# Kernel tuning notes

Measured on AMD Instinct MI355X. Metric: run time of the kernel, lower is better.

## Reference

```python
import jax, jax.numpy as jnp
import numpy as np


def _lerp_idx(in_size, out_size):
    # align_corners=True mapping: src = dst * (in-1)/(out-1)
    pos = jnp.arange(out_size, dtype=jnp.float32) * ((in_size - 1) / (out_size - 1))
    i0 = jnp.clip(jnp.floor(pos).astype(jnp.int32), 0, in_size - 2)
    w = pos - i0.astype(jnp.float32)
    return i0, i0 + 1, w


def _upsample_bilinear_ac(x, scale):
    # x: [B,C,H,W] -> [B,C,H*scale,W*scale], separable bilinear, align_corners=True
    B, C, H, W = x.shape
    Ho, Wo = H * scale, W * scale
    i0, i1, wy = _lerp_idx(H, Ho)
    j0, j1, wx = _lerp_idx(W, Wo)
    wy = wy[None, None, :, None]
    rows = x[:, :, i0, :] * (1.0 - wy) + x[:, :, i1, :] * wy  # [B,C,Ho,W]
    wx = wx[None, None, None, :]
    return rows[:, :, :, j0] * (1.0 - wx) + rows[:, :, :, j1] * wx  # [B,C,Ho,Wo]


def setup_inputs() -> dict:
    key = jax.random.key(0)
    k1, k2, k3 = jax.random.split(key, 3)
    x = jax.random.normal(k1, (4, 64, 96, 320), dtype=jnp.float32)
    weight = jax.random.normal(k2, (1, 64, 1, 1), dtype=jnp.float32) * 0.125
    bias = jax.random.normal(k3, (1,), dtype=jnp.float32) * 0.1
    return {"x": x, "weight": weight, "bias": bias}


def reference(x, weight, bias):
    SCALE = 4
    up = _upsample_bilinear_ac(x, SCALE)                     # [B,C,Ho,Wo]
    w2 = weight[:, :, 0, 0]                                   # [1,C]
    y = jnp.einsum('bchw,oc->bohw', up, w2) + bias[None, :, None, None]
    return jax.nn.relu(y)
```

## Files before the change

### kernel.cpp

```cpp
#include <hip/hip_runtime.h>


#define TH 32
#define TW 160
#define NR_MAX 10
#define NC_PAD 43

__global__ __launch_bounds__(256)
void UpsampleDepthOutputReLu_kernel(const float* __restrict__ x,
                                    const float* __restrict__ wgt,
                                    const float* __restrict__ bias,
                                    float* __restrict__ out)
{
    constexpr int C = 64, H = 96, W = 320, Ho = 384, Wo = 1280;
    const float RH = 95.0f / 383.0f;
    const float RW = 319.0f / 1279.0f;

    __shared__ float zs[NR_MAX * NC_PAD];
    __shared__ float ws[C];

    const int tid = threadIdx.x;
    const int b   = blockIdx.z;
    const int oh0 = blockIdx.y * TH;
    const int ow0 = blockIdx.x * TW;

    if (tid < C) ws[tid] = wgt[tid];

    const int i_lo  = min((int)((float)oh0 * RH), H - 2);
    const int i_hi  = min((int)((float)(oh0 + TH - 1) * RH), H - 2) + 1;
    const int nrows = i_hi - i_lo + 1;
    const int j_lo  = min((int)((float)ow0 * RW), W - 2);
    const int j_hi  = min((int)((float)(ow0 + TW - 1) * RW), W - 2) + 1;
    const int ncols = j_hi - j_lo + 1;

    __syncthreads();

    const int npatch = nrows * ncols;
    const float* xb = x + (size_t)b * C * H * W;
    for (int idx = tid; idx < npatch; idx += 256) {
        const int r = idx / ncols;
        const int c = idx - r * ncols;
        const float* p = xb + (size_t)(i_lo + r) * W + (j_lo + c);
        float acc = 0.f;
        #pragma unroll 16
        for (int ch = 0; ch < C; ++ch)
            acc += p[(size_t)ch * H * W] * ws[ch];
        zs[r * NC_PAD + c] = acc;
    }
    __syncthreads();

    const float bv = bias[0];
    float* ob = out + ((size_t)b * Ho + oh0) * Wo + ow0;
    #pragma unroll
    for (int k = 0; k < (TH * TW) / (256 * 4); ++k) {
        const int lin  = (k * 256 + tid) * 4;
        const int oh_l = lin / TW;
        const int ow_l = lin - oh_l * TW;

        const float ph = (float)(oh0 + oh_l) * RH;
        const int   i0 = min((int)ph, H - 2);
        const float wy = ph - (float)i0;
        const int   r  = i0 - i_lo;

        float vals[4];
        #pragma unroll
        for (int j = 0; j < 4; ++j) {
            const int   ow = ow0 + ow_l + j;
            const float pw = (float)ow * RW;
            const int   j0 = min((int)pw, W - 2);
            const float wx = pw - (float)j0;
            const int   c  = j0 - j_lo;
            const float top = zs[r * NC_PAD + c]       * (1.f - wx) + zs[r * NC_PAD + c + 1]       * wx;
            const float bot = zs[(r + 1) * NC_PAD + c] * (1.f - wx) + zs[(r + 1) * NC_PAD + c + 1] * wx;
            const float v   = top * (1.f - wy) + bot * wy + bv;
            vals[j] = fmaxf(v, 0.f);
        }
        *(float4*)(ob + (size_t)oh_l * Wo + ow_l) =
            make_float4(vals[0], vals[1], vals[2], vals[3]);
    }
}

extern "C" void kernel_launch(void* const* d_in, const int* in_sizes, int n_in,
                              void* d_out, int out_size, void* d_ws, size_t ws_size,
                              hipStream_t stream) {
    const float* x    = (const float*)d_in[0];
    const float* wgt  = (const float*)d_in[1];
    const float* bias = (const float*)d_in[2];
    float* out = (float*)d_out;

    dim3 grid(1280 / TW, 384 / TH, 4);
    UpsampleDepthOutputReLu_kernel<<<grid, 256, 0, stream>>>(x, wgt, bias, out);
}
```

Before: 84.03 us.

## Split into vectorized channel-reduce kernel and separate bilinear upsample kernel

Replaces the fused tiled kernel with two kernels: one reduces the 64 channels into a low-resolution map using float4 loads and a 4-lane shuffle reduction, storing it in workspace; a second performs bilinear upsampling, bias and ReLU from that map. This removes duplicated halo reductions and scalar strided loads in the fused kernel, aiming for better memory bandwidth on the dominant input read. It adds an extra launch and a small intermediate round trip through global memory.

```diff
diff --git a/kernel.cpp b/kernel.cpp
--- a/kernel.cpp
+++ b/kernel.cpp
@@ -1,83 +1,79 @@
 #include <hip/hip_runtime.h>
 
 
-#define TH 32
-#define TW 160
-#define NR_MAX 10
-#define NC_PAD 43
+constexpr int C = 64, H = 96, W = 320, HW = H * W;
+constexpr int Ho = 384, Wo = 1280;
+constexpr int HW4 = HW / 4;
 
 __global__ __launch_bounds__(256)
-void UpsampleDepthOutputReLu_kernel(const float* __restrict__ x,
-                                    const float* __restrict__ wgt,
-                                    const float* __restrict__ bias,
-                                    float* __restrict__ out)
+void reduce_c_kernel(const float* __restrict__ x,
+                     const float* __restrict__ wgt,
+                     float* __restrict__ z)
 {
-    constexpr int C = 64, H = 96, W = 320, Ho = 384, Wo = 1280;
+    __shared__ float ws[C];
+    const int tid = threadIdx.x;
+    if (tid < C) ws[tid] = wgt[tid];
+    __syncthreads();
+
+    const int gt = blockIdx.x * 256 + tid;
+    const int q  = gt >> 2;
+    const int lc = gt & 3;
+    const int b  = q / HW4;
+    const int s  = (q - b * HW4) * 4;
+
+    const float* p = x + (size_t)b * C * HW + s;
+    float4 acc = make_float4(0.f, 0.f, 0.f, 0.f);
+    #pragma unroll
+    for (int k = 0; k < 16; ++k) {
+        const int ch = lc * 16 + k;
+        const float4 v = *(const float4*)(p + (size_t)ch * HW);
+        const float wv = ws[ch];
+        acc.x += v.x * wv; acc.y += v.y * wv;
+        acc.z += v.z * wv; acc.w += v.w * wv;
+    }
+    acc.x += __shfl_xor(acc.x, 1); acc.y += __shfl_xor(acc.y, 1);
+    acc.z += __shfl_xor(acc.z, 1); acc.w += __shfl_xor(acc.w, 1);
+    acc.x += __shfl_xor(acc.x, 2); acc.y += __shfl_xor(acc.y, 2);
+    acc.z += __shfl_xor(acc.z, 2); acc.w += __shfl_xor(acc.w, 2);
+
+    if (lc == 0) ((float4*)z)[q] = acc;
+}
+
+__global__ __launch_bounds__(256)
+void upsample_kernel(const float* __restrict__ z,
+                     const float* __restrict__ bias,
+                     float* __restrict__ out)
+{
     const float RH = 95.0f / 383.0f;
     const float RW = 319.0f / 1279.0f;
 
-    __shared__ float zs[NR_MAX * NC_PAD];
-    __shared__ float ws[C];
+    const int gt = blockIdx.x * 256 + threadIdx.x;
+    const int o  = gt * 4;
+    const int b  = o / (Ho * Wo);
+    const int r  = o - b * (Ho * Wo);
+    const int oh = r / Wo;
+    const int ow = r - oh * Wo;
 
-    const int tid = threadIdx.x;
-    const int b   = blockIdx.z;
-    const int oh0 = blockIdx.y * TH;
-    const int ow0 = blockIdx.x * TW;
+    const float ph = (float)oh * RH;
+    const int   i0 = min((int)ph, H - 2);
+    const float wy = ph - (float)i0;
 
-    if (tid < C) ws[tid] = wgt[tid];
+    const float* z0 = z + ((size_t)b * H + i0) * W;
+    const float* z1 = z0 + W;
+    const float bv = bias[0];
 
-    const int i_lo  = min((int)((float)oh0 * RH), H - 2);
-    const int i_hi  = min((int)((float)(oh0 + TH - 1) * RH), H - 2) + 1;
-    const int nrows = i_hi - i_lo + 1;
-    const int j_lo  = min((int)((float)ow0 * RW), W - 2);
-    const int j_hi  = min((int)((float)(ow0 + TW - 1) * RW), W - 2) + 1;
-    const int ncols = j_hi - j_lo + 1;
-
-    __syncthreads();
-
-    const int npatch = nrows * ncols;
-    const float* xb = x + (size_t)b * C * H * W;
-    for (int idx = tid; idx < npatch; idx += 256) {
-        const int r = idx / ncols;
-        const int c = idx - r * ncols;
-        const float* p = xb + (size_t)(i_lo + r) * W + (j_lo + c);
-        float acc = 0.f;
-        #pragma unroll 16
-        for (int ch = 0; ch < C; ++ch)
-            acc += p[(size_t)ch * H * W] * ws[ch];
-        zs[r * NC_PAD + c] = acc;
+    float vals[4];
+    #pragma unroll
+    for (int j = 0; j < 4; ++j) {
+        const float pw = (float)(ow + j) * RW;
+        const int   j0 = min((int)pw, W - 2);
+        const float wx = pw - (float)j0;
+        const float top = z0[j0] * (1.f - wx) + z0[j0 + 1] * wx;
+        const float bot = z1[j0] * (1.f - wx) + z1[j0 + 1] * wx;
+        const float v   = top * (1.f - wy) + bot * wy + bv;
+        vals[j] = fmaxf(v, 0.f);
     }
-    __syncthreads();
-
-    const float bv = bias[0];
-    float* ob = out + ((size_t)b * Ho + oh0) * Wo + ow0;
-    #pragma unroll
-    for (int k = 0; k < (TH * TW) / (256 * 4); ++k) {
-        const int lin  = (k * 256 + tid) * 4;
-        const int oh_l = lin / TW;
-        const int ow_l = lin - oh_l * TW;
-
-        const float ph = (float)(oh0 + oh_l) * RH;
-        const int   i0 = min((int)ph, H - 2);
-        const float wy = ph - (float)i0;
-        const int   r  = i0 - i_lo;
-
-        float vals[4];
-        #pragma unroll
-        for (int j = 0; j < 4; ++j) {
-            const int   ow = ow0 + ow_l + j;
-            const float pw = (float)ow * RW;
-            const int   j0 = min((int)pw, W - 2);
-            const float wx = pw - (float)j0;
-            const int   c  = j0 - j_lo;
-            const float top = zs[r * NC_PAD + c]       * (1.f - wx) + zs[r * NC_PAD + c + 1]       * wx;
-            const float bot = zs[(r + 1) * NC_PAD + c] * (1.f - wx) + zs[(r + 1) * NC_PAD + c + 1] * wx;
-            const float v   = top * (1.f - wy) + bot * wy + bv;
-            vals[j] = fmaxf(v, 0.f);
-        }
-        *(float4*)(ob + (size_t)oh_l * Wo + ow_l) =
-            make_float4(vals[0], vals[1], vals[2], vals[3]);
-    }
+    ((float4*)out)[gt] = make_float4(vals[0], vals[1], vals[2], vals[3]);
 }
 
 extern "C" void kernel_launch(void* const* d_in, const int* in_sizes, int n_in,
@@ -87,7 +83,8 @@
     const float* wgt  = (const float*)d_in[1];
     const float* bias = (const float*)d_in[2];
     float* out = (float*)d_out;
+    float* z   = (float*)d_ws;
 
-    dim3 grid(1280 / TW, 384 / TH, 4);
-    UpsampleDepthOutputReLu_kernel<<<grid, 256, 0, stream>>>(x, wgt, bias, out);
+    reduce_c_kernel<<<dim3((4 * HW4 * 4) / 256), 256, 0, stream>>>(x, wgt, z);
+    upsample_kernel<<<dim3((4 * Ho * Wo / 4) / 256), 256, 0, stream>>>(z, bias, out);
 }
```

After: 81.32 us. 1.03x faster.
